# Optimization experiments

Measured on AMD Instinct MI355X. Metric: run time of the kernel, lower is better.

## Reference

```python
import jax, jax.numpy as jnp
import numpy as np

K = 16          # k_neighbors
C = 1.0         # Poincare ball curvature
ALPHA = 0.1     # residual blend strength
EPS = 1e-5


def poincare_project(x, c=C):
    # clip points to lie strictly inside the ball of radius 1/sqrt(c)
    norm = jnp.linalg.norm(x, axis=-1, keepdims=True)
    max_norm = (1.0 - EPS) / jnp.sqrt(c)
    scale = jnp.where(norm > max_norm, max_norm / jnp.maximum(norm, EPS), 1.0)
    return x * scale


def poincare_cdist(x, y, c=C):
    # x: [Nq, d], y: [M, d] -> [Nq, M] pairwise Poincare-ball distances
    x2 = jnp.sum(x * x, axis=-1)                       # [Nq]
    y2 = jnp.sum(y * y, axis=-1)                       # [M]
    xy = x @ y.T                                       # [Nq, M]
    sq = jnp.maximum(x2[:, None] + y2[None, :] - 2.0 * xy, 0.0)
    denom = (1.0 - c * x2)[:, None] * (1.0 - c * y2)[None, :]
    arg = 1.0 + 2.0 * c * sq / jnp.maximum(denom, EPS)
    return jnp.arccosh(jnp.maximum(arg, 1.0 + EPS)) / jnp.sqrt(c)


def layernorm(x, g, b):
    mu = jnp.mean(x, axis=-1, keepdims=True)
    var = jnp.var(x, axis=-1, keepdims=True)
    return (x - mu) * jax.lax.rsqrt(var + EPS) * g + b


def setup_inputs() -> dict:
    key = jax.random.key(0)
    ks = jax.random.split(key, 6)
    Nq, H, D, M = 2048, 1024, 256, 65536
    s1 = 1.0 / np.sqrt(H)
    s2 = 1.0 / np.sqrt(D)
    return {
        "hidden": jax.random.normal(ks[0], (Nq, H), jnp.float32),
        "memory": jax.random.normal(ks[1], (M, D), jnp.float32) * 0.1,
        "w1": jax.random.normal(ks[2], (H, D), jnp.float32) * s1,
        "b1": jnp.zeros((D,), jnp.float32),
        "ln_g": jnp.ones((D,), jnp.float32),
        "ln_b": jnp.zeros((D,), jnp.float32),
        "w2": jax.random.normal(ks[3], (D, D), jnp.float32) * s2,
        "b2": jnp.zeros((D,), jnp.float32),
        "wp": jax.random.normal(ks[4], (D, H), jnp.float32) * s2,
        "bp": jnp.zeros((H,), jnp.float32),
    }


def reference(hidden, memory, w1, b1, ln_g, ln_b, w2, b2, wp, bp):
    # query network: Linear -> LayerNorm -> GELU(exact) -> Linear
    q = layernorm(hidden @ w1 + b1, ln_g, ln_b)
    q = jax.nn.gelu(q, approximate=False) @ w2 + b2          # [Nq, D]

    # project query and memory bank onto the Poincare ball
    q_b = poincare_project(q)
    m_b = poincare_project(memory)

    # hyperbolic kNN: full pairwise distances, then top-k smallest
    dist = poincare_cdist(q_b, m_b)                          # [Nq, M]
    neg_topk, idx = jax.lax.top_k(-dist, K)                  # [Nq, K]

    # distance-weighted aggregation of retrieved memories
    w = jax.nn.softmax(neg_topk, axis=-1)                    # softmax(-dist)
    retrieved = jnp.einsum("nk,nkd->nd", w, m_b[idx])        # [Nq, D]

    # project back to hidden space, residual blend
    out = hidden + ALPHA * (retrieved @ wp + bp)             # [Nq, H]
    return out
```

## Files before the change

### kernel.cpp

```cpp
#include <hip/hip_runtime.h>
#include <hip/hip_bf16.h>

typedef unsigned int u32;
typedef unsigned short u16;
typedef unsigned char u8;
typedef __attribute__((ext_vector_type(8))) short short8;
typedef __attribute__((ext_vector_type(4))) float f32x4;
typedef __attribute__((ext_vector_type(4))) int i32x4;
typedef __attribute__((ext_vector_type(8))) int i32x8;

#define EPSV 1e-5f
#define MAXN (1.0f - 1e-5f)
#define THETA 0.17f
#define CAP 512
#define LCAPW 512u

__device__ __forceinline__ u16 f2bf(float f) {
    union { float f; u32 u; } v; v.f = f;
    u32 u = v.u;
    u32 r = (u + 0x7fffu + ((u >> 16) & 1u)) >> 16;
    return (u16)r;
}
__device__ __forceinline__ float bf2f(u16 h) {
    union { u32 u; float f; } v; v.u = ((u32)h) << 16;
    return v.f;
}
__device__ __forceinline__ u32 pk_fp8x4(float a, float b, float c, float d) {
    int v = __builtin_amdgcn_cvt_pk_fp8_f32(a, b, 0, false);
    v = __builtin_amdgcn_cvt_pk_fp8_f32(c, d, v, true);
    return (u32)v;
}
__device__ __forceinline__ u8 f2fp8(float a) {
    return (u8)(__builtin_amdgcn_cvt_pk_fp8_f32(a, a, 0, false) & 0xFF);
}

typedef __attribute__((address_space(1))) const unsigned char gbuf_t;
typedef __attribute__((address_space(3))) unsigned char lbuf_t;
__device__ __forceinline__ void gl2lds16(const void* g, void* l) {
    __builtin_amdgcn_global_load_lds((gbuf_t*)g, (lbuf_t*)l, 16, 0, 0);
}

__global__ __launch_bounds__(256) void k_pre(const float* __restrict__ mem,
                                             u16* __restrict__ mbf,
                                             u8* __restrict__ mbf8,
                                             float* __restrict__ y2m,
                                             u32* __restrict__ cnt,
                                             const float* __restrict__ hidden, u16* __restrict__ hb,
                                             const float* __restrict__ w1, u16* __restrict__ w1t,
                                             const float* __restrict__ w2, u16* __restrict__ w2t,
                                             const float* __restrict__ wp, u16* __restrict__ wpt) {
    __shared__ float ld[64 * 65];
    const int b = blockIdx.x, t = threadIdx.x;
    if (b < 16384) {
        int zi = b * 256 + t;
        if (zi < 2048) cnt[zi] = 0;
        const int row = b * 4 + (t >> 6);
        const int lane = t & 63;
        const float4* p = (const float4*)(mem + (size_t)row * 256);
        float4 v = p[lane];
        float ss = v.x * v.x + v.y * v.y + v.z * v.z + v.w * v.w;
#pragma unroll
        for (int off = 32; off; off >>= 1) ss += __shfl_xor(ss, off);
        float norm = sqrtf(ss);
        float scale = (norm > MAXN) ? MAXN / fmaxf(norm, EPSV) : 1.0f;
        float x0 = v.x * scale, x1 = v.y * scale, x2 = v.z * scale, x3 = v.w * scale;
        ushort4 u;
        u.x = f2bf(x0); u.y = f2bf(x1); u.z = f2bf(x2); u.w = f2bf(x3);
        *(ushort4*)&mbf[(size_t)row * 256 + lane * 4] = u;
        *(u32*)&mbf8[(size_t)row * 256 + lane * 4] = pk_fp8x4(x0, x1, x2, x3);
        if (lane == 0) y2m[row] = ss * scale * scale;
    } else if (b < 18432) {
        int i = (b - 16384) * 256 + t;
        float4 v = ((const float4*)hidden)[i];
        ushort4 u; u.x = f2bf(v.x); u.y = f2bf(v.y); u.z = f2bf(v.z); u.w = f2bf(v.w);
        ((ushort4*)hb)[i] = u;
    } else {
        const float* src; u16* dst; int K, N, tile;
        int bb = b - 18432;
        if (bb < 64)      { src = w1; dst = w1t; K = 1024; N = 256;  tile = bb; }
        else if (bb < 80) { src = w2; dst = w2t; K = 256;  N = 256;  tile = bb - 64; }
        else              { src = wp; dst = wpt; K = 256;  N = 1024; tile = bb - 80; }
        int ntn = N >> 6;
        int tk = (tile / ntn) * 64, tn = (tile - (tile / ntn) * ntn) * 64;
#pragma unroll
        for (int j = 0; j < 16; ++j) {
            int lin = j * 256 + t;
            int r = lin >> 6, c = lin & 63;
            ld[r * 65 + c] = src[(size_t)(tk + r) * N + tn + c];
        }
        __syncthreads();
#pragma unroll
        for (int j = 0; j < 16; ++j) {
            int lin = j * 256 + t;
            int c2 = lin >> 6, r2 = lin & 63;
            dst[(size_t)(tn + c2) * K + tk + r2] = f2bf(ld[r2 * 65 + c2]);
        }
    }
}

__global__ __launch_bounds__(256) void k_qnet(const u16* __restrict__ hb,
                                              const u16* __restrict__ w1t,
                                              const float* __restrict__ b1,
                                              const float* __restrict__ lng,
                                              const float* __restrict__ lnb,
                                              const u16* __restrict__ w2t,
                                              const float* __restrict__ b2,
                                              u8* __restrict__ qb8,
                                              float* __restrict__ x2q) {
    __shared__ float sm[16 * 260];
    __shared__ u16 qs[16 * 264];
    const int t = threadIdx.x;
    const int w = t >> 6, lane = t & 63;
    const int l16 = lane & 15, kq = (lane >> 4) * 8, rbase = (lane >> 4) * 4;
    const int q0 = blockIdx.x * 16;
    f32x4 zero = {0.f, 0.f, 0.f, 0.f};

    {
        f32x4 acc[4] = {zero, zero, zero, zero};
        const u16* ap = hb + (size_t)(q0 + l16) * 1024 + kq;
        for (int k0 = 0; k0 < 1024; k0 += 32) {
            short8 av = *(const short8*)(ap + k0);
#pragma unroll
            for (int ct = 0; ct < 4; ++ct) {
                int n = w * 64 + ct * 16 + l16;
                short8 bv = *(const short8*)&w1t[(size_t)n * 1024 + k0 + kq];
                acc[ct] = __builtin_amdgcn_mfma_f32_16x16x32_bf16(av, bv, acc[ct], 0, 0, 0);
            }
        }
#pragma unroll
        for (int ct = 0; ct < 4; ++ct) {
            int n = w * 64 + ct * 16 + l16;
            float bias = b1[n];
#pragma unroll
            for (int r = 0; r < 4; ++r)
                sm[(rbase + r) * 260 + n] = acc[ct][r] + bias;
        }
    }
    __syncthreads();
    {
        const int row = t >> 4, sub = t & 15;
        float s1 = 0.f, s2 = 0.f;
#pragma unroll
        for (int i = 0; i < 16; ++i) {
            float v = sm[row * 260 + sub + 16 * i];
            s1 += v; s2 += v * v;
        }
#pragma unroll
        for (int off = 8; off; off >>= 1) {
            s1 += __shfl_xor(s1, off, 16);
            s2 += __shfl_xor(s2, off, 16);
        }
        float mu = s1 * (1.0f / 256.0f);
        float var = s2 * (1.0f / 256.0f) - mu * mu;
        float rstd = rsqrtf(var + EPSV);
#pragma unroll
        for (int i = 0; i < 16; ++i) {
            int cc = sub + 16 * i;
            float v = sm[row * 260 + cc];
            float xn = (v - mu) * rstd * lng[cc] + lnb[cc];
            float ge = 0.5f * xn * (1.0f + erff(xn * 0.7071067811865475f));
            qs[row * 264 + cc] = f2bf(ge);
        }
    }
    __syncthreads();
    f32x4 acc2[4] = {zero, zero, zero, zero};
    for (int k0 = 0; k0 < 256; k0 += 32) {
        short8 av = *(const short8*)&qs[l16 * 264 + k0 + kq];
#pragma unroll
        for (int ct = 0; ct < 4; ++ct) {
            int n = w * 64 + ct * 16 + l16;
            short8 bv = *(const short8*)&w2t[(size_t)n * 256 + k0 + kq];
            acc2[ct] = __builtin_amdgcn_mfma_f32_16x16x32_bf16(av, bv, acc2[ct], 0, 0, 0);
        }
    }
    __syncthreads();
#pragma unroll
    for (int ct = 0; ct < 4; ++ct) {
        int n = w * 64 + ct * 16 + l16;
        float bias = b2[n];
#pragma unroll
        for (int r = 0; r < 4; ++r)
            sm[(rbase + r) * 260 + n] = acc2[ct][r] + bias;
    }
    __syncthreads();
    {
        const int row = t >> 4, sub = t & 15;
        float s2 = 0.f;
#pragma unroll
        for (int i = 0; i < 16; ++i) {
            float v = sm[row * 260 + sub + 16 * i];
            s2 += v * v;
        }
#pragma unroll
        for (int off = 8; off; off >>= 1) s2 += __shfl_xor(s2, off, 16);
        float norm = sqrtf(s2);
        float scale = (norm > MAXN) ? MAXN / fmaxf(norm, EPSV) : 1.0f;
        if (sub == 0) x2q[q0 + row] = s2 * scale * scale;
#pragma unroll
        for (int i = 0; i < 16; ++i) {
            int cc = sub + 16 * i;
            qb8[(size_t)(q0 + row) * 256 + cc] = f2fp8(sm[row * 260 + cc] * scale);
        }
    }
}

__global__ __launch_bounds__(256, 3) void k_dist(const u8* __restrict__ qb8,
                                                 const u8* __restrict__ mbf8,
                                                 u32* __restrict__ cnt,
                                                 uint2* __restrict__ cand) {
    __shared__ __align__(16) u8 ring[32768];
    __shared__ uint2 candW[4 * LCAPW];
    __shared__ u32 wcntS[4];
    const int b = blockIdx.x;
    const int xcd = b & 7;
    const int idx = b >> 3;
    const int qt = idx >> 1;
    const int mg = xcd * 2 + (idx & 1);
    const int q0 = qt * 64;
    const int m0 = mg * 4096;
    const int t = threadIdx.x;
    const int w = t >> 6, lane = t & 63;
    const int l16 = lane & 15, Q = lane >> 4, rbase = Q * 4;
    const int wn = w;

#pragma unroll
    for (int j = 0; j < 4; ++j) {
        int s = j * 256 + t;
        int r = s >> 4, p = s & 15;
        int c = p ^ (r & 15);
        gl2lds16(qb8 + (size_t)(q0 + r) * 256 + c * 16, ring + s * 16);
    }
    __syncthreads();

    i32x8 av[4][2];
#pragma unroll
    for (int i = 0; i < 4; ++i) {
        int R = i * 16 + l16;
        int aoff = R * 256 + (((Q * 2) ^ l16) << 4);
#pragma unroll
        for (int st = 0; st < 2; ++st) {
            i32x4 lo = *(const i32x4*)(ring + (aoff ^ (st << 7)));
            i32x4 hi = *(const i32x4*)(ring + (aoff ^ (st << 7) ^ 16));
            av[i][st] = __builtin_shufflevector(lo, hi, 0, 1, 2, 3, 4, 5, 6, 7);
        }
    }
    __syncthreads();

    const int rl = (lane >> 4);
    const int pch = lane & 15;
    const u8* pB[4];
#pragma unroll
    for (int i = 0; i < 4; ++i) {
        int rr = i * 4 + rl;
        int c = pch ^ rr;
        pB[i] = mbf8 + (size_t)(m0 + wn * 16 + rr) * 256 + c * 16;
    }
    u8* const wring = ring + w * 8192;
    const int ldst = lane * 16;

#pragma unroll
    for (int i = 0; i < 4; ++i) gl2lds16(pB[i], wring + i * 1024 + ldst);
#pragma unroll
    for (int i = 0; i < 4; ++i) gl2lds16(pB[i] + 16384, wring + 4096 + i * 1024 + ldst);

    const int boff = l16 * 256 + (((Q * 2) ^ l16) << 4);

    f32x4 zero = {0.f, 0.f, 0.f, 0.f};
    u32 wcnt = 0;
    const u32 mgbase = (u32)(m0 + wn * 16 + l16);

#pragma unroll 1
    for (int mt = 0; mt < 64; ++mt) {
        if (mt < 63) { asm volatile("s_waitcnt vmcnt(4)" ::: "memory"); }
        else         { asm volatile("s_waitcnt vmcnt(0)" ::: "memory"); }
        const u8* bufp = wring + ((mt & 1) << 12);
        i32x4 r00 = *(const i32x4*)(bufp + boff);
        i32x4 r01 = *(const i32x4*)(bufp + (boff ^ 16));
        i32x4 r10 = *(const i32x4*)(bufp + (boff ^ 128));
        i32x4 r11 = *(const i32x4*)(bufp + (boff ^ 128 ^ 16));
        asm volatile("s_waitcnt lgkmcnt(0)" ::: "memory");
        __builtin_amdgcn_sched_barrier(0);
        if (mt < 62) {
            const size_t so = (size_t)(mt + 2) * 16384;
            u8* d = (u8*)bufp;
#pragma unroll
            for (int i = 0; i < 4; ++i) gl2lds16(pB[i] + so, d + i * 1024 + ldst);
        }
        i32x8 bv0 = __builtin_shufflevector(r00, r01, 0, 1, 2, 3, 4, 5, 6, 7);
        i32x8 bv1 = __builtin_shufflevector(r10, r11, 0, 1, 2, 3, 4, 5, 6, 7);
        f32x4 acc[4] = {zero, zero, zero, zero};
#pragma unroll
        for (int i = 0; i < 4; ++i)
            acc[i] = __builtin_amdgcn_mfma_scale_f32_16x16x128_f8f6f4(
                av[i][0], bv0, acc[i], 0, 0, 0, 0x7F7F7F7F, 0, 0x7F7F7F7F);
#pragma unroll
        for (int i = 0; i < 4; ++i)
            acc[i] = __builtin_amdgcn_mfma_scale_f32_16x16x128_f8f6f4(
                av[i][1], bv1, acc[i], 0, 0, 0, 0x7F7F7F7F, 0, 0x7F7F7F7F);
        const u32 mglob = mgbase + (u32)(mt * 64);
#pragma unroll
        for (int i = 0; i < 4; ++i)
#pragma unroll
            for (int r = 0; r < 4; ++r) {
                float d = acc[i][r];
                unsigned long long mask = __ballot(d > THETA);
                if (mask) {
                    if (d > THETA) {
                        u32 pos = wcnt + (u32)__popcll(mask & ((1ull << lane) - 1ull));
                        if (pos < LCAPW)
                            candW[w * LCAPW + pos] =
                                make_uint2(((u32)(i * 16 + rbase + r) << 16) | mglob,
                                           __float_as_uint(d));
                    }
                    wcnt += (u32)__popcll(mask);
                }
            }
    }

    if (lane == 0) wcntS[w] = wcnt;
    __syncthreads();
#pragma unroll 1
    for (int wv = 0; wv < 4; ++wv) {
        u32 n = wcntS[wv]; if (n > LCAPW) n = LCAPW;
        for (u32 i = (u32)t; i < n; i += 256u) {
            uint2 e = candW[wv * LCAPW + i];
            int q = q0 + (int)(e.x >> 16);
            u32 pos = atomicAdd(&cnt[q], 1u);
            if (pos < CAP) cand[(size_t)q * CAP + pos] = make_uint2(e.x & 0xFFFFu, e.y);
        }
    }
}

__global__ __launch_bounds__(64, 4) void k_merge(const u32* __restrict__ cnt,
                                                 const uint2* __restrict__ cand,
                                                 const float* __restrict__ x2q,
                                                 const float* __restrict__ y2m,
                                                 const u16* __restrict__ mbf,
                                                 u16* __restrict__ rb) {
    const int q = blockIdx.x;
    const int lane = threadIdx.x;
    int n = (int)cnt[q]; if (n > CAP) n = CAP;
    const float x2 = x2q[q];
    const float dx = 1.0f - x2;
    float rv[8]; u32 mi[8];
#pragma unroll
    for (int j = 0; j < 8; ++j) {
        int idx = lane + 64 * j;
        rv[j] = 3.0e38f; mi[j] = 0;
        if (idx < n) {
            uint2 c = cand[(size_t)q * CAP + idx];
            float dot = __uint_as_float(c.y);
            float y2 = y2m[c.x];
            float sq = fmaxf(x2 + y2 - 2.0f * dot, 0.0f);
            float den = fmaxf(dx * (1.0f - y2), EPSV);
            rv[j] = sq / den;
            mi[j] = c.x;
        }
    }
    __shared__ float sdist[16];
    __shared__ u32 smi[16];
    __shared__ float swt[16];
    for (int k = 0; k < 16; ++k) {
        float lm = rv[0]; int ls = 0;
#pragma unroll
        for (int j = 1; j < 8; ++j) if (rv[j] < lm) { lm = rv[j]; ls = j; }
        unsigned long long key = (((unsigned long long)__float_as_uint(lm)) << 32) | (u32)(lane * 8 + ls);
#pragma unroll
        for (int off = 32; off; off >>= 1) {
            unsigned long long o = __shfl_xor(key, off);
            key = (o < key) ? o : key;
        }
        u32 sid = (u32)(key & 0xffffffffu);
        int wl = (int)(sid >> 3), wslot = (int)(sid & 7);
        if (lane == wl) {
            sdist[k] = rv[wslot];
            smi[k] = mi[wslot];
            rv[wslot] = 3.0e38f;
        }
    }
    __syncthreads();
    float rr = sdist[lane & 15];
    float arg = fmaxf(fmaf(2.0f, rr, 1.0f), 1.0f + EPSV);
    float dneg = -acoshf(arg);
    float mx = dneg;
#pragma unroll
    for (int off = 8; off; off >>= 1) mx = fmaxf(mx, __shfl_xor(mx, off, 16));
    float e = expf(dneg - mx);
    float ssum = e;
#pragma unroll
    for (int off = 8; off; off >>= 1) ssum += __shfl_xor(ssum, off, 16);
    if (lane < 16) swt[lane] = e / ssum;
    __syncthreads();
    float acc[4] = {0.f, 0.f, 0.f, 0.f};
    for (int k = 0; k < 16; ++k) {
        float wk = swt[k];
        const u16* mr = mbf + (size_t)smi[k] * 256;
#pragma unroll
        for (int j = 0; j < 4; ++j) acc[j] += wk * bf2f(mr[lane + 64 * j]);
    }
#pragma unroll
    for (int j = 0; j < 4; ++j) rb[(size_t)q * 256 + lane + 64 * j] = f2bf(acc[j]);
}

__global__ __launch_bounds__(256) void k_out(const u16* __restrict__ rb,
                                             const u16* __restrict__ wpt,
                                             const float* __restrict__ bp,
                                             const float* __restrict__ hidden,
                                             float* __restrict__ out) {
    const int b = blockIdx.x;
    const int mt = b & 31, nt = b >> 5;
    const int t = threadIdx.x;
    const int w = t >> 6, lane = t & 63;
    const int l16 = lane & 15, kq = (lane >> 4) * 8, rbase = (lane >> 4) * 4;
    const int n = nt * 64 + w * 16 + l16;
    f32x4 zero = {0.f, 0.f, 0.f, 0.f};
    f32x4 acc[4] = {zero, zero, zero, zero};
    for (int k0 = 0; k0 < 256; k0 += 32) {
        short8 bv = *(const short8*)&wpt[(size_t)n * 256 + k0 + kq];
#pragma unroll
        for (int rt = 0; rt < 4; ++rt) {
            short8 av = *(const short8*)&rb[(size_t)(mt * 64 + rt * 16 + l16) * 256 + k0 + kq];
            acc[rt] = __builtin_amdgcn_mfma_f32_16x16x32_bf16(av, bv, acc[rt], 0, 0, 0);
        }
    }
    float bpn = bp[n];
#pragma unroll
    for (int rt = 0; rt < 4; ++rt)
#pragma unroll
        for (int r = 0; r < 4; ++r) {
            int m = mt * 64 + rt * 16 + rbase + r;
            out[(size_t)m * 1024 + n] = hidden[(size_t)m * 1024 + n] + 0.1f * (acc[rt][r] + bpn);
        }
}

extern "C" void kernel_launch(void* const* d_in, const int* in_sizes, int n_in,
                              void* d_out, int out_size, void* d_ws, size_t ws_size,
                              hipStream_t stream) {
    const float* hidden = (const float*)d_in[0];
    const float* memory = (const float*)d_in[1];
    const float* w1 = (const float*)d_in[2];
    const float* b1 = (const float*)d_in[3];
    const float* ln_g = (const float*)d_in[4];
    const float* ln_b = (const float*)d_in[5];
    const float* w2 = (const float*)d_in[6];
    const float* b2 = (const float*)d_in[7];
    const float* wp = (const float*)d_in[8];
    const float* bp = (const float*)d_in[9];
    float* out = (float*)d_out;
    char* ws = (char*)d_ws;

    u16* mbf  = (u16*)(ws);
    float* y2m = (float*)(ws + 33554432);
    u16* hb   = (u16*)(ws + 33816576);
    u16* w1t  = (u16*)(ws + 38010880);
    u16* w2t  = (u16*)(ws + 38535168);
    u16* wpt  = (u16*)(ws + 38666240);
    u8*  qb8  = (u8*)(ws + 40239104);
    float* x2q = (float*)(ws + 41287680);
    u32* cnt  = (u32*)(ws + 41295872);
    uint2* cand = (uint2*)(ws + 41304064);
    u16* rb   = (u16*)(ws + 49692672);
    u8*  mbf8 = (u8*)(ws + 50741248);

    hipLaunchKernelGGL(k_pre, dim3(18576), dim3(256), 0, stream,
                       memory, mbf, mbf8, y2m, cnt, hidden, hb, w1, w1t, w2, w2t, wp, wpt);
    hipLaunchKernelGGL(k_qnet, dim3(128), dim3(256), 0, stream,
                       hb, w1t, b1, ln_g, ln_b, w2t, b2, qb8, x2q);
    hipLaunchKernelGGL(k_dist, dim3(512), dim3(256), 0, stream, qb8, mbf8, cnt, cand);
    hipLaunchKernelGGL(k_merge, dim3(2048), dim3(64), 0, stream, cnt, cand, x2q, y2m, mbf, rb);
    hipLaunchKernelGGL(k_out, dim3(512), dim3(256), 0, stream, rb, wpt, bp, hidden, out);
}
```

Before: 272.1 us.

## Widen per-wave memory tile to 32 rows in distance kernel

Each wave now processes 32 memory rows per iteration instead of 16. The LDS ring is doubled to 64KB, each prefetch stage issues 8 async loads instead of 4, and the loop runs half as many iterations. Each B-tile load now feeds twice as many MFMAs, which halves per-iteration loop, wait and barrier overhead relative to compute and improves A-fragment reuse. In exchange, LDS use roughly doubles, occupancy drops from 3 to 2 blocks per CU, and the per-wave candidate buffer shrinks to 384 entries, which raises overflow risk.

```diff
diff --git a/kernel.cpp b/kernel.cpp
--- a/kernel.cpp
+++ b/kernel.cpp
@@ -13,7 +13,7 @@
 #define MAXN (1.0f - 1e-5f)
 #define THETA 0.17f
 #define CAP 512
-#define LCAPW 512u
+#define LCAPW 384u
 
 __device__ __forceinline__ u16 f2bf(float f) {
     union { float f; u32 u; } v; v.f = f;
@@ -204,11 +204,11 @@
     }
 }
 
-__global__ __launch_bounds__(256, 3) void k_dist(const u8* __restrict__ qb8,
+__global__ __launch_bounds__(256, 2) void k_dist(const u8* __restrict__ qb8,
                                                  const u8* __restrict__ mbf8,
                                                  u32* __restrict__ cnt,
                                                  uint2* __restrict__ cand) {
-    __shared__ __align__(16) u8 ring[32768];
+    __shared__ __align__(16) u8 ring[65536];
     __shared__ uint2 candW[4 * LCAPW];
     __shared__ u32 wcntS[4];
     const int b = blockIdx.x;
@@ -221,7 +221,6 @@
     const int t = threadIdx.x;
     const int w = t >> 6, lane = t & 63;
     const int l16 = lane & 15, Q = lane >> 4, rbase = Q * 4;
-    const int wn = w;
 
 #pragma unroll
     for (int j = 0; j < 4; ++j) {
@@ -248,73 +247,91 @@
 
     const int rl = (lane >> 4);
     const int pch = lane & 15;
-    const u8* pB[4];
-#pragma unroll
-    for (int i = 0; i < 4; ++i) {
+    const u8* pB[8];
+#pragma unroll
+    for (int i = 0; i < 8; ++i) {
         int rr = i * 4 + rl;
-        int c = pch ^ rr;
-        pB[i] = mbf8 + (size_t)(m0 + wn * 16 + rr) * 256 + c * 16;
-    }
-    u8* const wring = ring + w * 8192;
+        int c = pch ^ (rr & 15);
+        pB[i] = mbf8 + (size_t)(m0 + w * 32 + rr) * 256 + c * 16;
+    }
+    u8* const wring = ring + w * 16384;
     const int ldst = lane * 16;
 
 #pragma unroll
-    for (int i = 0; i < 4; ++i) gl2lds16(pB[i], wring + i * 1024 + ldst);
-#pragma unroll
-    for (int i = 0; i < 4; ++i) gl2lds16(pB[i] + 16384, wring + 4096 + i * 1024 + ldst);
-
-    const int boff = l16 * 256 + (((Q * 2) ^ l16) << 4);
+    for (int i = 0; i < 8; ++i) gl2lds16(pB[i], wring + i * 1024 + ldst);
+#pragma unroll
+    for (int i = 0; i < 8; ++i) gl2lds16(pB[i] + 32768, wring + 8192 + i * 1024 + ldst);
+
+    const int boff0 = l16 * 256 + (((Q * 2) ^ l16) << 4);
+    const int boff1 = boff0 + 4096;
 
     f32x4 zero = {0.f, 0.f, 0.f, 0.f};
     u32 wcnt = 0;
-    const u32 mgbase = (u32)(m0 + wn * 16 + l16);
+    const u32 mgbase = (u32)(m0 + w * 32 + l16);
 
 #pragma unroll 1
-    for (int mt = 0; mt < 64; ++mt) {
-        if (mt < 63) { asm volatile("s_waitcnt vmcnt(4)" ::: "memory"); }
+    for (int mt = 0; mt < 32; ++mt) {
+        if (mt < 31) { asm volatile("s_waitcnt vmcnt(8)" ::: "memory"); }
         else         { asm volatile("s_waitcnt vmcnt(0)" ::: "memory"); }
-        const u8* bufp = wring + ((mt & 1) << 12);
-        i32x4 r00 = *(const i32x4*)(bufp + boff);
-        i32x4 r01 = *(const i32x4*)(bufp + (boff ^ 16));
-        i32x4 r10 = *(const i32x4*)(bufp + (boff ^ 128));
-        i32x4 r11 = *(const i32x4*)(bufp + (boff ^ 128 ^ 16));
+        const u8* bufp = wring + ((mt & 1) << 13);
+        i32x4 a00 = *(const i32x4*)(bufp + boff0);
+        i32x4 a01 = *(const i32x4*)(bufp + (boff0 ^ 16));
+        i32x4 a10 = *(const i32x4*)(bufp + (boff0 ^ 128));
+        i32x4 a11 = *(const i32x4*)(bufp + (boff0 ^ 128 ^ 16));
+        i32x4 c00 = *(const i32x4*)(bufp + boff1);
+        i32x4 c01 = *(const i32x4*)(bufp + (boff1 ^ 16));
+        i32x4 c10 = *(const i32x4*)(bufp + (boff1 ^ 128));
+        i32x4 c11 = *(const i32x4*)(bufp + (boff1 ^ 128 ^ 16));
         asm volatile("s_waitcnt lgkmcnt(0)" ::: "memory");
         __builtin_amdgcn_sched_barrier(0);
-        if (mt < 62) {
-            const size_t so = (size_t)(mt + 2) * 16384;
+        if (mt < 30) {
+            const size_t so = (size_t)(mt + 2) * 32768;
             u8* d = (u8*)bufp;
 #pragma unroll
-            for (int i = 0; i < 4; ++i) gl2lds16(pB[i] + so, d + i * 1024 + ldst);
-        }
-        i32x8 bv0 = __builtin_shufflevector(r00, r01, 0, 1, 2, 3, 4, 5, 6, 7);
-        i32x8 bv1 = __builtin_shufflevector(r10, r11, 0, 1, 2, 3, 4, 5, 6, 7);
-        f32x4 acc[4] = {zero, zero, zero, zero};
+            for (int i = 0; i < 8; ++i) gl2lds16(pB[i] + so, d + i * 1024 + ldst);
+        }
+        i32x8 bv00 = __builtin_shufflevector(a00, a01, 0, 1, 2, 3, 4, 5, 6, 7);
+        i32x8 bv10 = __builtin_shufflevector(a10, a11, 0, 1, 2, 3, 4, 5, 6, 7);
+        i32x8 bv01 = __builtin_shufflevector(c00, c01, 0, 1, 2, 3, 4, 5, 6, 7);
+        i32x8 bv11 = __builtin_shufflevector(c10, c11, 0, 1, 2, 3, 4, 5, 6, 7);
+        f32x4 acc[4][2];
+#pragma unroll
+        for (int i = 0; i < 4; ++i) { acc[i][0] = zero; acc[i][1] = zero; }
+#pragma unroll
+        for (int i = 0; i < 4; ++i) {
+            acc[i][0] = __builtin_amdgcn_mfma_scale_f32_16x16x128_f8f6f4(
+                av[i][0], bv00, acc[i][0], 0, 0, 0, 0x7F7F7F7F, 0, 0x7F7F7F7F);
+            acc[i][1] = __builtin_amdgcn_mfma_scale_f32_16x16x128_f8f6f4(
+                av[i][0], bv01, acc[i][1], 0, 0, 0, 0x7F7F7F7F, 0, 0x7F7F7F7F);
+        }
+#pragma unroll
+        for (int i = 0; i < 4; ++i) {
+            acc[i][0] = __builtin_amdgcn_mfma_scale_f32_16x16x128_f8f6f4(
+                av[i][1], bv10, acc[i][0], 0, 0, 0, 0x7F7F7F7F, 0, 0x7F7F7F7F);
+            acc[i][1] = __builtin_amdgcn_mfma_scale_f32_16x16x128_f8f6f4(
+                av[i][1], bv11, acc[i][1], 0, 0, 0, 0x7F7F7F7F, 0, 0x7F7F7F7F);
+        }
+        const u32 mglob = mgbase + (u32)(mt * 128);
 #pragma unroll
         for (int i = 0; i < 4; ++i)
-            acc[i] = __builtin_amdgcn_mfma_scale_f32_16x16x128_f8f6f4(
-                av[i][0], bv0, acc[i], 0, 0, 0, 0x7F7F7F7F, 0, 0x7F7F7F7F);
-#pragma unroll
-        for (int i = 0; i < 4; ++i)
-            acc[i] = __builtin_amdgcn_mfma_scale_f32_16x16x128_f8f6f4(
-                av[i][1], bv1, acc[i], 0, 0, 0, 0x7F7F7F7F, 0, 0x7F7F7F7F);
-        const u32 mglob = mgbase + (u32)(mt * 64);
-#pragma unroll
-        for (int i = 0; i < 4; ++i)
-#pragma unroll
-            for (int r = 0; r < 4; ++r) {
-                float d = acc[i][r];
-                unsigned long long mask = __ballot(d > THETA);
-                if (mask) {
-                    if (d > THETA) {
-                        u32 pos = wcnt + (u32)__popcll(mask & ((1ull << lane) - 1ull));
-                        if (pos < LCAPW)
-                            candW[w * LCAPW + pos] =
-                                make_uint2(((u32)(i * 16 + rbase + r) << 16) | mglob,
-                                           __float_as_uint(d));
+#pragma unroll
+            for (int cf = 0; cf < 2; ++cf)
+#pragma unroll
+                for (int r = 0; r < 4; ++r) {
+                    float d = acc[i][cf][r];
+                    unsigned long long mask = __ballot(d > THETA);
+                    if (mask) {
+                        if (d > THETA) {
+                            u32 pos = wcnt + (u32)__popcll(mask & ((1ull << lane) - 1ull));
+                            if (pos < LCAPW)
+                                candW[w * LCAPW + pos] =
+                                    make_uint2(((u32)(i * 16 + rbase + r) << 16) |
+                                               (mglob + (u32)(cf * 16)),
+                                               __float_as_uint(d));
+                        }
+                        wcnt += (u32)__popcll(mask);
                     }
-                    wcnt += (u32)__popcll(mask);
                 }
-            }
     }
 
     if (lane == 0) wcntS[w] = wcnt;
```

New measurement: 264.9 us. 1.03x faster.
